# Optimization experiments

Measured on AMD Instinct MI355X. Metric: run time of the kernel, lower is better.

## Reference

```python
import jax, jax.numpy as jnp
import numpy as np

DIM = 256
B = 8
H = 56
W = 56
K = 2
EPS = 1e-5  # torch BatchNorm2d default eps


def _conv1x1(x, w, b):
    # x: [B,C,H,W], w: [O,C], b: [O]
    return jnp.einsum('oc,bchw->bohw', w, x) + b[None, :, None, None]


def _bn(x, g, be, m, v):
    # inference-mode BatchNorm2d with running stats
    s = g / jnp.sqrt(v + EPS)
    return x * s[None, :, None, None] + (be - m * s)[None, :, None, None]


def _grapher(x, w1, b1, g1, be1, m1, v1, wg, bg, gg, beg, mg, vg, w2, b2, g2, be2, m2, v2):
    # fc1: 1x1 conv + BN
    h = _bn(_conv1x1(x, w1, b1), g1, be1, m1, v1)
    Hh, Ww = h.shape[2], h.shape[3]
    # MRConv4d: running max over circular-shift differences
    # torch.cat([x[:,:,-i:,:], x[:,:,:-i,:]], dim=2) == jnp.roll(x, i, axis=2)
    xj = jnp.zeros_like(h)

    def body_h(c, i):
        return jnp.maximum(c, h - jnp.roll(h, i, axis=2)), None

    xj, _ = jax.lax.scan(body_h, xj, jnp.arange(K, Hh, K))

    def body_w(c, i):
        return jnp.maximum(c, h - jnp.roll(h, i, axis=3)), None

    xj, _ = jax.lax.scan(body_w, xj, jnp.arange(K, Ww, K))

    cat = jnp.concatenate([h, xj], axis=1)  # [B, 2*dim, H, W]
    # MRConv4d.nn: Conv2d(2*dim, 2*dim, 1) -> BN(2*dim) -> GELU (exact erf)
    g = jax.nn.gelu(_bn(_conv1x1(cat, wg, bg), gg, beg, mg, vg), approximate=False)
    # fc2: Conv2d(2*dim, dim, 1) + BN(dim), then residual
    return _bn(_conv1x1(g, w2, b2), g2, be2, m2, v2) + x


def setup_inputs() -> dict:
    key = jax.random.key(0)
    ks = jax.random.split(key, 12)
    d, d2 = DIM, 2 * DIM

    def w(k, o, c):
        return jax.random.normal(k, (o, c), jnp.float32) * np.float32(1.0 / np.sqrt(c))

    return {
        'x': jax.random.normal(ks[0], (B, d, H, W), jnp.float32),
        'w1': w(ks[1], d, d), 'b1': jnp.zeros((d,), jnp.float32),
        'g1': jnp.ones((d,), jnp.float32), 'be1': jnp.zeros((d,), jnp.float32),
        'm1': jax.random.normal(ks[2], (d,), jnp.float32) * 0.1,
        'v1': jax.random.uniform(ks[3], (d,), jnp.float32, 0.5, 1.5),
        'wg': w(ks[4], d2, d2), 'bg': jnp.zeros((d2,), jnp.float32),
        'gg': jnp.ones((d2,), jnp.float32), 'beg': jnp.zeros((d2,), jnp.float32),
        'mg': jax.random.normal(ks[5], (d2,), jnp.float32) * 0.1,
        'vg': jax.random.uniform(ks[6], (d2,), jnp.float32, 0.5, 1.5),
        'w2': w(ks[7], d, d2), 'b2': jnp.zeros((d,), jnp.float32),
        'g2': jnp.ones((d,), jnp.float32), 'be2': jnp.zeros((d,), jnp.float32),
        'm2': jax.random.normal(ks[8], (d,), jnp.float32) * 0.1,
        'v2': jax.random.uniform(ks[9], (d,), jnp.float32, 0.5, 1.5),
    }


def reference(x, w1, b1, g1, be1, m1, v1, wg, bg, gg, beg, mg, vg, w2, b2, g2, be2, m2, v2):
    return _grapher(x, w1, b1, g1, be1, m1, v1, wg, bg, gg, beg, mg, vg, w2, b2, g2, be2, m2, v2)
```

## Files before the change

### kernel.cpp

```cpp
#include <hip/hip_runtime.h>
#include <math.h>

#define SPB 3136
#define NB 8
#define EPS 1e-5f

typedef unsigned short u16;
typedef __attribute__((ext_vector_type(8))) short short8;
typedef __attribute__((ext_vector_type(4))) float float4v;

__device__ __forceinline__ float b2f(u16 v){ unsigned u=((unsigned)v)<<16; float f; __builtin_memcpy(&f,&u,4); return f; }
__device__ __forceinline__ u16 f2b(float f){ unsigned u; __builtin_memcpy(&u,&f,4); u += 0x7fffu + ((u>>16)&1u); return (u16)(u>>16); }
__device__ __forceinline__ float gelu_f(float z){ return 0.5f*z*(1.0f+erff(z*0.70710678118654752f)); }

__global__ void prep_consts_k(const float* b1,const float* g1,const float* be1,const float* m1,const float* v1,
                              const float* bg,const float* gg,const float* beg,const float* mg,const float* vg,
                              const float* b2,const float* g2,const float* be2,const float* m2,const float* v2,
                              float* cst){
  int i = threadIdx.x;
  if (i < 256) {
    float s = g1[i]*rsqrtf(v1[i]+EPS);
    cst[i] = s; cst[256+i] = b1[i]*s + be1[i] - m1[i]*s;
    float s2 = g2[i]*rsqrtf(v2[i]+EPS);
    cst[1536+i] = s2; cst[1792+i] = b2[i]*s2 + be2[i] - m2[i]*s2;
  }
  float s = gg[i]*rsqrtf(vg[i]+EPS);
  cst[512+i] = s; cst[1024+i] = bg[i]*s + beg[i] - mg[i]*s;
}

__global__ void conv_w_k(const float* __restrict__ w1,const float* __restrict__ wg,const float* __restrict__ w2,
                         u16* __restrict__ w1b,u16* __restrict__ wgb,u16* __restrict__ w2b){
  int i = blockIdx.x*256 + threadIdx.x;
  if (i < 65536)  w1b[i] = f2b(w1[i]);
  if (i < 262144) wgb[i] = f2b(wg[i]);
  if (i < 131072) w2b[i] = f2b(w2[i]);
}

__global__ void transpose_x_k(const float* __restrict__ x, u16* __restrict__ xt){
  __shared__ float t[32][33];
  int b = blockIdx.z, ct = blockIdx.y, st = blockIdx.x;
  int ts = threadIdx.x, tc = threadIdx.y;
  #pragma unroll
  for (int i=0;i<4;i++){
    int c = tc + i*8;
    t[c][ts] = x[((size_t)(b*256 + ct*32 + c))*SPB + st*32 + ts];
  }
  __syncthreads();
  #pragma unroll
  for (int i=0;i<4;i++){
    int r = tc + i*8;
    xt[((size_t)(b*SPB + st*32 + r))*256 + ct*32 + ts] = f2b(t[ts][r]);
  }
}

__global__ void rowmin_k(const u16* __restrict__ cat, float* __restrict__ rmin){
  int b = blockIdx.x/56, y = blockIdx.x%56, c = threadIdx.x;
  float mE=3.4e38f, mO=3.4e38f;
  const u16* base = cat + ((size_t)(b*SPB + y*56))*512 + c;
  for (int x=0;x<56;x+=2){
    mE = fminf(mE, b2f(base[(size_t)x*512]));
    mO = fminf(mO, b2f(base[(size_t)(x+1)*512]));
  }
  rmin[((size_t)(b*2+0)*56 + y)*256 + c]=mE;
  rmin[((size_t)(b*2+1)*56 + y)*256 + c]=mO;
}
__global__ void colmin_k(const u16* __restrict__ cat, float* __restrict__ cmin){
  int b = blockIdx.x/56, x = blockIdx.x%56, c = threadIdx.x;
  float mE=3.4e38f, mO=3.4e38f;
  const u16* base = cat + ((size_t)(b*SPB + x))*512 + c;
  for (int y=0;y<56;y+=2){
    mE = fminf(mE, b2f(base[(size_t)(y*56)*512]));
    mO = fminf(mO, b2f(base[(size_t)((y+1)*56)*512]));
  }
  cmin[((size_t)(b*2+0)*56 + x)*256 + c]=mE;
  cmin[((size_t)(b*2+1)*56 + x)*256 + c]=mO;
}
__global__ void xj_k(u16* __restrict__ cat, const float* __restrict__ rmin, const float* __restrict__ cmin){
  int b = blockIdx.y, s = blockIdx.x, c = threadIdx.x;
  int y = s/56, x = s%56;
  size_t idx = ((size_t)(b*SPB + s))*512;
  float h = b2f(cat[idx + c]);
  float m = fminf(cmin[((size_t)(b*2+(y&1))*56 + x)*256 + c],
                  rmin[((size_t)(b*2+(x&1))*56 + y)*256 + c]);
  cat[idx + 256 + c] = f2b(fmaxf(0.0f, h - m));
}

template<int KTOT, int EPI>
__global__ __launch_bounds__(256) void gemm_k(
    const u16* __restrict__ Ain, const u16* __restrict__ Wt,
    const float* __restrict__ scale, const float* __restrict__ bias,
    void* __restrict__ outp, const float* __restrict__ resid)
{
  __shared__ __align__(16) u16 smem[8192];
  u16* As = smem;
  u16* Bs = smem + 64*40;
  const int tid = threadIdx.x;
  const int b = blockIdx.z;
  const int s0 = blockIdx.x * 64;
  const int o0 = blockIdx.y * 128;
  const int lane = tid & 63, wid = tid >> 6;
  const int quad = lane >> 4, l16 = lane & 15;
  const int wm = wid & 1, wn = wid >> 1;

  float4v acc[2][4];
  #pragma unroll
  for (int i=0;i<2;i++)
    #pragma unroll
    for (int j=0;j<4;j++) acc[i][j] = (float4v){0.f,0.f,0.f,0.f};

  const int arow = tid >> 2, aoff = (tid & 3)*8;
  const u16* Ab  = Ain + ((size_t)(b*SPB + s0 + arow))*KTOT + aoff;
  const u16* Wb0 = Wt + ((size_t)(o0 + arow))*KTOT + aoff;
  const u16* Wb1 = Wt + ((size_t)(o0 + 64 + arow))*KTOT + aoff;
  u16* Asw  = As + arow*40 + aoff;
  u16* Bsw0 = Bs + arow*40 + aoff;
  u16* Bsw1 = Bs + (64+arow)*40 + aoff;

  for (int kt = 0; kt < KTOT; kt += 32) {
    *(uint4*)Asw  = *(const uint4*)(Ab + kt);
    *(uint4*)Bsw0 = *(const uint4*)(Wb0 + kt);
    *(uint4*)Bsw1 = *(const uint4*)(Wb1 + kt);
    __syncthreads();
    short8 af[2], bfr[4];
    #pragma unroll
    for (int im=0;im<2;im++) af[im] = *(const short8*)&As[(wm*32+im*16+l16)*40 + quad*8];
    #pragma unroll
    for (int in=0;in<4;in++) bfr[in] = *(const short8*)&Bs[(wn*64+in*16+l16)*40 + quad*8];
    #pragma unroll
    for (int im=0;im<2;im++)
      #pragma unroll
      for (int in=0;in<4;in++)
        acc[im][in] = __builtin_amdgcn_mfma_f32_16x16x32_bf16(af[im], bfr[in], acc[im][in], 0, 0, 0);
    __syncthreads();
  }

  if (EPI == 1 || EPI == 2) {
    u16* tile = smem;
    #pragma unroll
    for (int im=0;im<2;im++)
      #pragma unroll
      for (int in=0;in<4;in++){
        int ol = wn*64 + in*16 + l16;
        float sc = scale[o0+ol], bi = bias[o0+ol];
        #pragma unroll
        for (int r=0;r<4;r++){
          float v = acc[im][in][r]*sc + bi;
          if (EPI==2) v = gelu_f(v);
          tile[(wm*32+im*16+quad*4+r)*128 + ol] = f2b(v);
        }
      }
    __syncthreads();
    u16* op = (u16*)outp;
    #pragma unroll
    for (int p=0;p<4;p++){
      int chunk = p*256 + tid;
      int row = chunk >> 4, off = (chunk & 15)*8;
      *(uint4*)&op[((size_t)(b*SPB + s0 + row))*512 + o0 + off] = *(const uint4*)&tile[row*128 + off];
    }
  } else {
    float* ftile = (float*)smem;
    float* op = (float*)outp;
    #pragma unroll
    for (int h=0; h<2; h++){
      if (wn == h){
        #pragma unroll
        for (int im=0;im<2;im++)
          #pragma unroll
          for (int in=0;in<4;in++){
            int ol = in*16 + l16;
            int og = o0 + wn*64 + ol;
            float sc = scale[og], bi = bias[og];
            float4v v;
            #pragma unroll
            for (int r=0;r<4;r++) v[r] = acc[im][in][r]*sc + bi;
            *(float4v*)&ftile[ol*64 + wm*32 + im*16 + quad*4] = v;
          }
      }
      __syncthreads();
      #pragma unroll
      for (int p=0;p<4;p++){
        int chunk = p*256 + tid;
        int row = chunk >> 4, off = (chunk & 15)*4;
        size_t g = ((size_t)(b*256 + o0 + h*64 + row))*SPB + s0 + off;
        float4v v = *(const float4v*)&ftile[row*64 + off];
        v.x += resid[g]; v.y += resid[g+1]; v.z += resid[g+2]; v.w += resid[g+3];
        *(float4v*)&op[g] = v;
      }
      __syncthreads();
    }
  }
}

extern "C" void kernel_launch(void* const* d_in, const int* in_sizes, int n_in,
                              void* d_out, int out_size, void* d_ws, size_t ws_size,
                              hipStream_t stream)
{
  const float* x  = (const float*)d_in[0];
  const float* w1 = (const float*)d_in[1];
  const float* b1 = (const float*)d_in[2];
  const float* g1 = (const float*)d_in[3];
  const float* be1= (const float*)d_in[4];
  const float* m1 = (const float*)d_in[5];
  const float* v1 = (const float*)d_in[6];
  const float* wg = (const float*)d_in[7];
  const float* bg = (const float*)d_in[8];
  const float* gg = (const float*)d_in[9];
  const float* beg= (const float*)d_in[10];
  const float* mg = (const float*)d_in[11];
  const float* vg = (const float*)d_in[12];
  const float* w2 = (const float*)d_in[13];
  const float* b2 = (const float*)d_in[14];
  const float* g2 = (const float*)d_in[15];
  const float* be2= (const float*)d_in[16];
  const float* m2 = (const float*)d_in[17];
  const float* v2 = (const float*)d_in[18];

  char* ws = (char*)d_ws;
  size_t off = 0;
  auto alloc = [&](size_t bytes){ void* p = ws + off; off += (bytes + 255) & ~(size_t)255; return p; };
  u16* xt    = (u16*)alloc((size_t)NB*SPB*256*2);
  u16* catt  = (u16*)alloc((size_t)NB*SPB*512*2);
  u16* gt    = (u16*)alloc((size_t)NB*SPB*512*2);
  u16* w1b   = (u16*)alloc((size_t)65536*2);
  u16* wgb   = (u16*)alloc((size_t)262144*2);
  u16* w2b   = (u16*)alloc((size_t)131072*2);
  float* cst = (float*)alloc((size_t)2048*4);
  float* rmin= (float*)alloc((size_t)NB*2*56*256*4);
  float* cmin= (float*)alloc((size_t)NB*2*56*256*4);

  hipLaunchKernelGGL(prep_consts_k, dim3(1), dim3(512), 0, stream,
                     b1,g1,be1,m1,v1, bg,gg,beg,mg,vg, b2,g2,be2,m2,v2, cst);
  hipLaunchKernelGGL(conv_w_k, dim3(1024), dim3(256), 0, stream, w1,wg,w2, w1b,wgb,w2b);
  hipLaunchKernelGGL(transpose_x_k, dim3(98,8,8), dim3(32,8), 0, stream, x, xt);
  hipLaunchKernelGGL((gemm_k<256,1>), dim3(49,2,8), dim3(256), 0, stream,
                     xt, w1b, cst+0, cst+256, (void*)catt, (const float*)nullptr);
  hipLaunchKernelGGL(rowmin_k, dim3(NB*56), dim3(256), 0, stream, catt, rmin);
  hipLaunchKernelGGL(colmin_k, dim3(NB*56), dim3(256), 0, stream, catt, cmin);
  hipLaunchKernelGGL(xj_k, dim3(SPB, NB), dim3(256), 0, stream, catt, rmin, cmin);
  hipLaunchKernelGGL((gemm_k<512,2>), dim3(49,4,8), dim3(256), 0, stream,
                     catt, wgb, cst+512, cst+1024, (void*)gt, (const float*)nullptr);
  hipLaunchKernelGGL((gemm_k<512,3>), dim3(49,2,8), dim3(256), 0, stream,
                     gt, w2b, cst+1536, cst+1792, d_out, x);
}
```

Baseline: 211.0 us.

## Enlarge GEMM M-tile to 128 over flattened batch and load tiles directly into LDS

```diff
diff --git a/kernel.cpp b/kernel.cpp
--- a/kernel.cpp
+++ b/kernel.cpp
@@ -3,6 +3,7 @@
 
 #define SPB 3136
 #define NB 8
+#define MTOT (NB*SPB)
 #define EPS 1e-5f
 
 typedef unsigned short u16;
@@ -12,6 +13,11 @@
 __device__ __forceinline__ float b2f(u16 v){ unsigned u=((unsigned)v)<<16; float f; __builtin_memcpy(&f,&u,4); return f; }
 __device__ __forceinline__ u16 f2b(float f){ unsigned u; __builtin_memcpy(&u,&f,4); u += 0x7fffu + ((u>>16)&1u); return (u16)(u>>16); }
 __device__ __forceinline__ float gelu_f(float z){ return 0.5f*z*(1.0f+erff(z*0.70710678118654752f)); }
+
+__device__ __forceinline__ void gll16(const u16* g, u16* l){
+  __builtin_amdgcn_global_load_lds((const __attribute__((address_space(1))) void*)g,
+                                   (__attribute__((address_space(3))) void*)l, 16, 0, 0);
+}
 
 __global__ void prep_consts_k(const float* b1,const float* g1,const float* be1,const float* m1,const float* v1,
                               const float* bg,const float* gg,const float* beg,const float* mg,const float* vg,
@@ -91,43 +97,45 @@
     const float* __restrict__ scale, const float* __restrict__ bias,
     void* __restrict__ outp, const float* __restrict__ resid)
 {
-  __shared__ __align__(16) u16 smem[8192];
+  __shared__ __align__(16) u16 smem[16896];
   u16* As = smem;
-  u16* Bs = smem + 64*40;
+  u16* Bs = smem + 4096;
   const int tid = threadIdx.x;
-  const int b = blockIdx.z;
-  const int s0 = blockIdx.x * 64;
+  const int m0 = blockIdx.x * 128;
   const int o0 = blockIdx.y * 128;
   const int lane = tid & 63, wid = tid >> 6;
   const int quad = lane >> 4, l16 = lane & 15;
   const int wm = wid & 1, wn = wid >> 1;
 
-  float4v acc[2][4];
+  float4v acc[4][4];
   #pragma unroll
-  for (int i=0;i<2;i++)
+  for (int i=0;i<4;i++)
     #pragma unroll
     for (int j=0;j<4;j++) acc[i][j] = (float4v){0.f,0.f,0.f,0.f};
 
-  const int arow = tid >> 2, aoff = (tid & 3)*8;
-  const u16* Ab  = Ain + ((size_t)(b*SPB + s0 + arow))*KTOT + aoff;
-  const u16* Wb0 = Wt + ((size_t)(o0 + arow))*KTOT + aoff;
-  const u16* Wb1 = Wt + ((size_t)(o0 + 64 + arow))*KTOT + aoff;
-  u16* Asw  = As + arow*40 + aoff;
-  u16* Bsw0 = Bs + arow*40 + aoff;
-  u16* Bsw1 = Bs + (64+arow)*40 + aoff;
+  const int row = tid >> 2, q8 = (tid & 3) * 8;
+  const u16* ga0 = Ain + ((size_t)(m0 + row))*KTOT + q8;
+  const u16* ga1 = ga0 + (size_t)64*KTOT;
+  const u16* gb0 = Wt  + ((size_t)(o0 + row))*KTOT + q8;
+  const u16* gb1 = gb0 + (size_t)64*KTOT;
+  u16* la0 = As + tid*8;
+  u16* la1 = As + 2048 + tid*8;
+  u16* lb0 = Bs + tid*8;
+  u16* lb1 = Bs + 2048 + tid*8;
 
   for (int kt = 0; kt < KTOT; kt += 32) {
-    *(uint4*)Asw  = *(const uint4*)(Ab + kt);
-    *(uint4*)Bsw0 = *(const uint4*)(Wb0 + kt);
-    *(uint4*)Bsw1 = *(const uint4*)(Wb1 + kt);
+    gll16(ga0 + kt, la0);
+    gll16(ga1 + kt, la1);
+    gll16(gb0 + kt, lb0);
+    gll16(gb1 + kt, lb1);
     __syncthreads();
-    short8 af[2], bfr[4];
-    #pragma unroll
-    for (int im=0;im<2;im++) af[im] = *(const short8*)&As[(wm*32+im*16+l16)*40 + quad*8];
-    #pragma unroll
-    for (int in=0;in<4;in++) bfr[in] = *(const short8*)&Bs[(wn*64+in*16+l16)*40 + quad*8];
-    #pragma unroll
-    for (int im=0;im<2;im++)
+    short8 af[4], bfr[4];
+    #pragma unroll
+    for (int im=0;im<4;im++) af[im]  = *(const short8*)&As[(wm*64+im*16+l16)*32 + quad*8];
+    #pragma unroll
+    for (int in=0;in<4;in++) bfr[in] = *(const short8*)&Bs[(wn*64+in*16+l16)*32 + quad*8];
+    #pragma unroll
+    for (int im=0;im<4;im++)
       #pragma unroll
       for (int in=0;in<4;in++)
         acc[im][in] = __builtin_amdgcn_mfma_f32_16x16x32_bf16(af[im], bfr[in], acc[im][in], 0, 0, 0);
@@ -137,7 +145,7 @@
   if (EPI == 1 || EPI == 2) {
     u16* tile = smem;
     #pragma unroll
-    for (int im=0;im<2;im++)
+    for (int im=0;im<4;im++)
       #pragma unroll
       for (int in=0;in<4;in++){
         int ol = wn*64 + in*16 + l16;
@@ -146,16 +154,16 @@
         for (int r=0;r<4;r++){
           float v = acc[im][in][r]*sc + bi;
           if (EPI==2) v = gelu_f(v);
-          tile[(wm*32+im*16+quad*4+r)*128 + ol] = f2b(v);
+          tile[(wm*64+im*16+quad*4+r)*128 + ol] = f2b(v);
         }
       }
     __syncthreads();
     u16* op = (u16*)outp;
     #pragma unroll
-    for (int p=0;p<4;p++){
+    for (int p=0;p<8;p++){
       int chunk = p*256 + tid;
-      int row = chunk >> 4, off = (chunk & 15)*8;
-      *(uint4*)&op[((size_t)(b*SPB + s0 + row))*512 + o0 + off] = *(const uint4*)&tile[row*128 + off];
+      int rr = chunk >> 4, off = (chunk & 15)*8;
+      *(uint4*)&op[((size_t)(m0 + rr))*512 + o0 + off] = *(const uint4*)&tile[rr*128 + off];
     }
   } else {
     float* ftile = (float*)smem;
@@ -164,25 +172,27 @@
     for (int h=0; h<2; h++){
       if (wn == h){
         #pragma unroll
-        for (int im=0;im<2;im++)
+        for (int im=0;im<4;im++)
           #pragma unroll
           for (int in=0;in<4;in++){
-            int ol = in*16 + l16;
-            int og = o0 + wn*64 + ol;
+            int c64 = in*16 + l16;
+            int og = o0 + h*64 + c64;
             float sc = scale[og], bi = bias[og];
             float4v v;
             #pragma unroll
             for (int r=0;r<4;r++) v[r] = acc[im][in][r]*sc + bi;
-            *(float4v*)&ftile[ol*64 + wm*32 + im*16 + quad*4] = v;
+            *(float4v*)&ftile[c64*132 + wm*64 + im*16 + quad*4] = v;
           }
       }
       __syncthreads();
       #pragma unroll
-      for (int p=0;p<4;p++){
+      for (int p=0;p<8;p++){
         int chunk = p*256 + tid;
-        int row = chunk >> 4, off = (chunk & 15)*4;
-        size_t g = ((size_t)(b*256 + o0 + h*64 + row))*SPB + s0 + off;
-        float4v v = *(const float4v*)&ftile[row*64 + off];
+        int rr = chunk >> 5, off = (chunk & 31)*4;
+        int m = m0 + off;
+        int b = m / SPB, s = m - b*SPB;
+        size_t g = ((size_t)(b*256 + o0 + h*64 + rr))*SPB + s;
+        float4v v = *(const float4v*)&ftile[rr*132 + off];
         v.x += resid[g]; v.y += resid[g+1]; v.z += resid[g+2]; v.w += resid[g+3];
         *(float4v*)&op[g] = v;
       }
@@ -218,9 +228,9 @@
   char* ws = (char*)d_ws;
   size_t off = 0;
   auto alloc = [&](size_t bytes){ void* p = ws + off; off += (bytes + 255) & ~(size_t)255; return p; };
-  u16* xt    = (u16*)alloc((size_t)NB*SPB*256*2);
-  u16* catt  = (u16*)alloc((size_t)NB*SPB*512*2);
-  u16* gt    = (u16*)alloc((size_t)NB*SPB*512*2);
+  u16* xt    = (u16*)alloc((size_t)MTOT*256*2);
+  u16* catt  = (u16*)alloc((size_t)MTOT*512*2);
+  u16* gt    = (u16*)alloc((size_t)MTOT*512*2);
   u16* w1b   = (u16*)alloc((size_t)65536*2);
   u16* wgb   = (u16*)alloc((size_t)262144*2);
   u16* w2b   = (u16*)alloc((size_t)131072*2);
@@ -232,13 +242,13 @@
                      b1,g1,be1,m1,v1, bg,gg,beg,mg,vg, b2,g2,be2,m2,v2, cst);
   hipLaunchKernelGGL(conv_w_k, dim3(1024), dim3(256), 0, stream, w1,wg,w2, w1b,wgb,w2b);
   hipLaunchKernelGGL(transpose_x_k, dim3(98,8,8), dim3(32,8), 0, stream, x, xt);
-  hipLaunchKernelGGL((gemm_k<256,1>), dim3(49,2,8), dim3(256), 0, stream,
+  hipLaunchKernelGGL((gemm_k<256,1>), dim3(196,2), dim3(256), 0, stream,
                      xt, w1b, cst+0, cst+256, (void*)catt, (const float*)nullptr);
   hipLaunchKernelGGL(rowmin_k, dim3(NB*56), dim3(256), 0, stream, catt, rmin);
   hipLaunchKernelGGL(colmin_k, dim3(NB*56), dim3(256), 0, stream, catt, cmin);
   hipLaunchKernelGGL(xj_k, dim3(SPB, NB), dim3(256), 0, stream, catt, rmin, cmin);
-  hipLaunchKernelGGL((gemm_k<512,2>), dim3(49,4,8), dim3(256), 0, stream,
+  hipLaunchKernelGGL((gemm_k<512,2>), dim3(196,4), dim3(256), 0, stream,
                      catt, wgb, cst+512, cst+1024, (void*)gt, (const float*)nullptr);
-  hipLaunchKernelGGL((gemm_k<512,3>), dim3(49,2,8), dim3(256), 0, stream,
+  hipLaunchKernelGGL((gemm_k<512,3>), dim3(196,2), dim3(256), 0, stream,
                      gt, w2b, cst+1536, cst+1792, d_out, x);
 }
```

After: 205.9 us. -2.4%, faster.
